# Performance work log

Measured on AMD Instinct MI355X. Metric: run time of the kernel, lower is better.

Reference implementation:

```python
import jax, jax.numpy as jnp
import numpy as np

B, S, D, H = 4, 2048, 1024, 16
DEPTH = D // H


def setup_inputs() -> dict:
    key = jax.random.key(0)
    ks = jax.random.split(key, 11)
    s = 1.0 / np.sqrt(D)
    return {
        "q": jax.random.normal(ks[0], (B, S, D), jnp.float32),
        "k": jax.random.normal(ks[1], (B, S, D), jnp.float32),
        "v": jax.random.normal(ks[2], (B, S, D), jnp.float32),
        "wq": jax.random.normal(ks[3], (D, D), jnp.float32) * s,
        "bq": jnp.zeros((D,), jnp.float32),
        "wk": jax.random.normal(ks[4], (D, D), jnp.float32) * s,
        "bk": jnp.zeros((D,), jnp.float32),
        "wv": jax.random.normal(ks[5], (D, D), jnp.float32) * s,
        "bv": jnp.zeros((D,), jnp.float32),
        "wo": jax.random.normal(ks[6], (D, D), jnp.float32) * s,
        "bo": jnp.zeros((D,), jnp.float32),
    }


def _split_heads(x):
    # [B,S,D] -> [B,H,S,depth]
    b, s, _ = x.shape
    return x.reshape(b, s, H, DEPTH).transpose(0, 2, 1, 3)


def reference(q, k, v, wq, bq, wk, bk, wv, bv, wo, bo):
    qh = _split_heads(q @ wq + bq)
    kh = _split_heads(k @ wk + bk)
    vh = _split_heads(v @ wv + bv)
    scale = 1.0 / jnp.sqrt(jnp.asarray(DEPTH, jnp.float32))
    logits = jnp.einsum("bhsd,bhtd->bhst", qh, kh) * scale  # [B,H,S,S]
    attn = jax.nn.softmax(logits, axis=-1)
    out = jnp.einsum("bhst,bhtd->bhsd", attn, vh)
    out = out.transpose(0, 2, 1, 3).reshape(q.shape[0], -1, D)
    return out @ wo + bo
```

## Files before the change

### kernel.cpp

```cpp
#include <hip/hip_runtime.h>
#include <hip/hip_bf16.h>

#define BATCH 4
#define SEQ   2048
#define DIM   1024
#define NHEAD 16
#define HDIM  64

typedef __bf16    bf16x8 __attribute__((ext_vector_type(8)));
typedef float     f32x16 __attribute__((ext_vector_type(16)));
typedef unsigned  u32;

__device__ __forceinline__ unsigned short f2bfu(float x) {
  union { __hip_bfloat16 b; unsigned short u; } c; c.b = __float2bfloat16(x); return c.u;
}
__device__ __forceinline__ u32 cvtpk(float lo, float hi) {
  u32 r; asm("v_cvt_pk_bf16_f32 %0, %1, %2" : "=v"(r) : "v"(lo), "v"(hi)); return r;
}
__device__ __forceinline__ int swz4(int row) {
  return ((row & 7) ^ ((row >> 3) & 7)) << 2;
}

#define GLDS16(GP, LP)                                                         \
  __builtin_amdgcn_global_load_lds(                                            \
      (const __attribute__((address_space(1))) void*)(GP),                     \
      (__attribute__((address_space(3))) void*)(LP), 16, 0, 0)

__global__ __launch_bounds__(256)
void wtrans(const float* __restrict__ w0, const float* __restrict__ w1,
            const float* __restrict__ w2,
            __hip_bfloat16* __restrict__ t0, __hip_bfloat16* __restrict__ t1,
            __hip_bfloat16* __restrict__ t2)
{
  __shared__ float T[64][68];
  const int mat  = blockIdx.x >> 8;
  const int tile = blockIdx.x & 255;
  const float* W = mat == 0 ? w0 : (mat == 1 ? w1 : w2);
  __hip_bfloat16* Wt = mat == 0 ? t0 : (mat == 1 ? t1 : t2);
  const int k0 = (tile >> 4) * 64, n0 = (tile & 15) * 64;
  const int tid = threadIdx.x;
  const int r = tid >> 2, cq = (tid & 3) * 16;
  #pragma unroll
  for (int j = 0; j < 4; ++j) {
    const float4 v = *reinterpret_cast<const float4*>(&W[(size_t)(k0 + r) * DIM + n0 + cq + j * 4]);
    T[r][cq + j * 4 + 0] = v.x; T[r][cq + j * 4 + 1] = v.y;
    T[r][cq + j * 4 + 2] = v.z; T[r][cq + j * 4 + 3] = v.w;
  }
  __syncthreads();
  u32 o[8];
  #pragma unroll
  for (int j = 0; j < 8; ++j)
    o[j] = cvtpk(T[cq + 2 * j][r], T[cq + 2 * j + 1][r]);
  *reinterpret_cast<uint4*>(&Wt[(size_t)(n0 + r) * DIM + k0 + cq + 0]) = make_uint4(o[0], o[1], o[2], o[3]);
  *reinterpret_cast<uint4*>(&Wt[(size_t)(n0 + r) * DIM + k0 + cq + 8]) = make_uint4(o[4], o[5], o[6], o[7]);
}

template<typename TIN, typename TOUT, int NSEG>
__global__ __launch_bounds__(256, 2)
void gemm2ph(const TIN* __restrict__ A0, const TIN* __restrict__ A1, const TIN* __restrict__ A2,
             const __hip_bfloat16* __restrict__ W0, const __hip_bfloat16* __restrict__ W1,
             const __hip_bfloat16* __restrict__ W2,
             const float* __restrict__ b0, const float* __restrict__ b1, const float* __restrict__ b2,
             TOUT* __restrict__ C0, TOUT* __restrict__ C1, TOUT* __restrict__ C2)
{
  __shared__ __align__(16) u32 As32[2][128][32];
  __shared__ __align__(16) u32 Bs32[2][128][32];

  constexpr bool AF32 = (sizeof(TIN) == 4);
  constexpr int K = 1024, NT = 16;

  const int seg = (NSEG == 1) ? 0 : (blockIdx.x >> 9);
  const int idb = (NSEG == 1) ? blockIdx.x : (blockIdx.x & 511);
  const TIN* A = seg == 0 ? A0 : (seg == 1 ? A1 : A2);
  const __hip_bfloat16* Wt = seg == 0 ? W0 : (seg == 1 ? W1 : W2);
  const float* bias = seg == 0 ? b0 : (seg == 1 ? b1 : b2);
  TOUT* C = seg == 0 ? C0 : (seg == 1 ? C1 : C2);

  const int xcd = idb & 7, rr = idb >> 3;
  const int bx = rr & 7, by = xcd + 8 * (rr >> 3);
  const int m0 = by * 128, n0 = bx * 128;

  const int tid = threadIdx.x, lane = tid & 63, w = tid >> 6;
  const int l31 = lane & 31, hi = lane >> 5;
  const int wm = w >> 1, wn = w & 1;

  f32x16 acc[2][2] = {};

  const __hip_bfloat16* bptr[4];
  #pragma unroll
  for (int i = 0; i < 4; ++i) {
    const int off = (w * 4 + i) * 1024 + lane * 16;
    const int r = off >> 7;
    const int s = (off >> 4) & 7;
    bptr[i] = Wt + (size_t)(n0 + r) * K + (s ^ (r & 7)) * 8;
  }
  const TIN* aptr[4];
  const int arow = tid >> 3;
  const int acb  = (tid & 7) * 8;
  #pragma unroll
  for (int i = 0; i < 4; ++i) {
    if constexpr (!AF32) {
      const int off = (w * 4 + i) * 1024 + lane * 16;
      const int r = off >> 7;
      const int s = (off >> 4) & 7;
      aptr[i] = A + (size_t)(m0 + r) * K + (s ^ (r & 7)) * 8;
    } else {
      aptr[i] = nullptr;
    }
  }

  float4 ar[4][2];

  auto loadA_f32 = [&](int t) {
    #pragma unroll
    for (int p = 0; p < 4; ++p) {
      const float* ap = (const float*)A + (size_t)(m0 + arow + p * 32) * K + t * 64 + acb;
      ar[p][0] = *reinterpret_cast<const float4*>(ap);
      ar[p][1] = *reinterpret_cast<const float4*>(ap + 4);
    }
  };
  auto writeA_f32 = [&](int nxt) {
    #pragma unroll
    for (int p = 0; p < 4; ++p) {
      const int row = arow + p * 32;
      uint4 pk;
      pk.x = cvtpk(ar[p][0].x, ar[p][0].y);
      pk.y = cvtpk(ar[p][0].z, ar[p][0].w);
      pk.z = cvtpk(ar[p][1].x, ar[p][1].y);
      pk.w = cvtpk(ar[p][1].z, ar[p][1].w);
      *reinterpret_cast<uint4*>(&As32[nxt][row][((tid & 7) * 4) ^ ((row & 7) << 2)]) = pk;
    }
  };
  auto stageA_bf = [&](int nxt, int t) {
    #pragma unroll
    for (int i = 0; i < 4; ++i)
      GLDS16((const __hip_bfloat16*)aptr[i] + t * 64,
             (char*)As32 + nxt * 16384 + (w * 4 + i) * 1024);
  };
  auto stageB = [&](int nxt, int t) {
    #pragma unroll
    for (int i = 0; i < 4; ++i)
      GLDS16(bptr[i] + t * 64,
             (char*)Bs32 + nxt * 16384 + (w * 4 + i) * 1024);
  };

  int aoff[4][2], boff[4][2];
  #pragma unroll
  for (int kk = 0; kk < 4; ++kk) {
    #pragma unroll
    for (int mi = 0; mi < 2; ++mi) {
      const int r = wm * 64 + mi * 32 + l31;
      aoff[kk][mi] = r * 128 + (((kk * 2 + hi) ^ (r & 7)) << 4);
    }
    #pragma unroll
    for (int ni = 0; ni < 2; ++ni) {
      const int c = wn * 64 + ni * 32 + l31;
      boff[kk][ni] = c * 128 + (((kk * 2 + hi) ^ (c & 7)) << 4);
    }
  }

  if constexpr (AF32) { loadA_f32(0); writeA_f32(0); }
  else                { stageA_bf(0, 0); }
  stageB(0, 0);
  __syncthreads();

  for (int t = 0; t < NT; ++t) {
    const int cur = t & 1, nxt = cur ^ 1;

    if (t + 1 < NT) {
      if constexpr (AF32) loadA_f32(t + 1);
      else                stageA_bf(nxt, t + 1);
      stageB(nxt, t + 1);
    }

    const char* ab = (const char*)As32 + cur * 16384;
    const char* bb = (const char*)Bs32 + cur * 16384;
    #pragma unroll
    for (int kk = 0; kk < 4; ++kk) {
      bf16x8 af[2], bfv[2];
      #pragma unroll
      for (int mi = 0; mi < 2; ++mi)
        af[mi] = *reinterpret_cast<const bf16x8*>(ab + aoff[kk][mi]);
      #pragma unroll
      for (int ni = 0; ni < 2; ++ni)
        bfv[ni] = *reinterpret_cast<const bf16x8*>(bb + boff[kk][ni]);
      __builtin_amdgcn_s_setprio(1);
      #pragma unroll
      for (int mi = 0; mi < 2; ++mi)
        #pragma unroll
        for (int ni = 0; ni < 2; ++ni)
          acc[mi][ni] = __builtin_amdgcn_mfma_f32_32x32x16_bf16(af[mi], bfv[ni], acc[mi][ni], 0, 0, 0);
      __builtin_amdgcn_s_setprio(0);
    }

    if (t + 1 < NT) {
      if constexpr (AF32) writeA_f32(nxt);
    }
    __syncthreads();
  }

  #pragma unroll
  for (int ni = 0; ni < 2; ++ni) {
    const int col = n0 + wn * 64 + ni * 32 + l31;
    const float bv = bias[col];
    #pragma unroll
    for (int mi = 0; mi < 2; ++mi) {
      #pragma unroll
      for (int g = 0; g < 4; ++g)
        #pragma unroll
        for (int e = 0; e < 4; ++e) {
          const int row = m0 + wm * 64 + mi * 32 + g * 8 + hi * 4 + e;
          const float val = acc[mi][ni][g * 4 + e] + bv;
          if constexpr (sizeof(TOUT) == 2)
            C[(size_t)row * DIM + col] = __float2bfloat16(val);
          else
            C[(size_t)row * DIM + col] = val;
        }
    }
  }
}

__global__ __launch_bounds__(256, 2)
void flash_attn(const __hip_bfloat16* __restrict__ Qb,
                const __hip_bfloat16* __restrict__ Kb,
                const __hip_bfloat16* __restrict__ Vb,
                __hip_bfloat16* __restrict__ Ob)
{
  __shared__ __align__(16) u32 Ks32[2][64][32];
  __shared__ __align__(16) u32 Vt32[2][64][32];

  const int id  = blockIdx.x;
  const int xcd = id & 7;
  const int r_  = id >> 3;
  const int qb  = r_ & 7;
  const int hh  = (r_ >> 3) & 1;
  const int b   = r_ >> 4;
  const int h   = xcd + 8 * hh;

  const int tid = threadIdx.x, lane = tid & 63, wv = tid >> 6;
  const int l31 = lane & 31, hi = lane >> 5;

  const size_t headoff = (size_t)h * HDIM;
  const int q0 = b * SEQ + qb * 256 + wv * 64;

  bf16x8 qf[2][4];
  #pragma unroll
  for (int qh = 0; qh < 2; ++qh)
    #pragma unroll
    for (int dk = 0; dk < 4; ++dk)
      qf[qh][dk] = *reinterpret_cast<const bf16x8*>(
        &Qb[(size_t)(q0 + qh * 32 + l31) * DIM + headoff + dk * 16 + hi * 8]);

  f32x16 accO[2][2] = {};
  float l_run[2] = {0.f, 0.f};

  const int skey = tid >> 2;
  const int sdq  = tid & 3;
  const int vkp  = tid >> 3;
  const int vdb  = tid & 7;
  const size_t kbase = (size_t)b * SEQ * DIM + headoff;

  uint4 kst[2], vst[2];
  auto load_t = [&](int t) {
    const int kb = t * 64;
    const __hip_bfloat16* kp_ = &Kb[kbase + (size_t)(kb + skey) * DIM + sdq * 16];
    kst[0] = *reinterpret_cast<const uint4*>(kp_);
    kst[1] = *reinterpret_cast<const uint4*>(kp_ + 8);
    const __hip_bfloat16* vp_ = &Vb[kbase + (size_t)(kb + vkp * 2) * DIM + vdb * 8];
    vst[0] = *reinterpret_cast<const uint4*>(vp_);
    vst[1] = *reinterpret_cast<const uint4*>(vp_ + DIM);
  };
  auto store_t = [&](int bb) {
    const int sk = swz4(skey);
    *reinterpret_cast<uint4*>(&Ks32[bb][skey][(sdq * 8 + 0) ^ sk]) = kst[0];
    *reinterpret_cast<uint4*>(&Ks32[bb][skey][(sdq * 8 + 4) ^ sk]) = kst[1];
    const unsigned short* a  = (const unsigned short*)&vst[0];
    const unsigned short* bv = (const unsigned short*)&vst[1];
    #pragma unroll
    for (int j = 0; j < 8; ++j) {
      const int row = vdb * 8 + j;
      Vt32[bb][row][vkp ^ swz4(row)] = (u32)a[j] | ((u32)bv[j] << 16);
    }
  };

  load_t(0); store_t(0); __syncthreads();

  const float C1 = 0.125f * 1.44269504f;

  for (int t = 0; t < SEQ / 64; ++t) {
    const int bb = t & 1;
    if (t < SEQ / 64 - 1) load_t(t + 1);

    f32x16 sacc[2][2] = {};
    __builtin_amdgcn_s_setprio(1);
    #pragma unroll
    for (int kt = 0; kt < 2; ++kt) {
      const int row = kt * 32 + l31;
      const int sk = swz4(row);
      #pragma unroll
      for (int dk = 0; dk < 4; ++dk) {
        bf16x8 kf = *reinterpret_cast<const bf16x8*>(&Ks32[bb][row][(dk * 8 + hi * 4) ^ sk]);
        sacc[0][kt] = __builtin_amdgcn_mfma_f32_32x32x16_bf16(kf, qf[0][dk], sacc[0][kt], 0, 0, 0);
        sacc[1][kt] = __builtin_amdgcn_mfma_f32_32x32x16_bf16(kf, qf[1][dk], sacc[1][kt], 0, 0, 0);
      }
    }
    __builtin_amdgcn_s_setprio(0);

    u32 pf[2][4][4];
    #pragma unroll
    for (int qh = 0; qh < 2; ++qh) {
      #pragma unroll
      for (int kt = 0; kt < 2; ++kt)
        #pragma unroll
        for (int r2 = 0; r2 < 16; ++r2)
          sacc[qh][kt][r2] = __builtin_amdgcn_exp2f(sacc[qh][kt][r2] * C1);

      f32x16 ps = sacc[qh][0] + sacc[qh][1];
      float s8[8];
      #pragma unroll
      for (int i = 0; i < 8; ++i) s8[i] = ps[i] + ps[i + 8];
      float rs = ((s8[0] + s8[1]) + (s8[2] + s8[3])) + ((s8[4] + s8[5]) + (s8[6] + s8[7]));
      rs += __shfl_xor(rs, 32);
      l_run[qh] += rs;

#define MAKE_PF(DST, P, B) do {                                            \
      u32 x1 = cvtpk(P[B+0], P[B+1]);                                      \
      u32 y1 = cvtpk(P[B+4], P[B+5]);                                      \
      u32 x2 = cvtpk(P[B+2], P[B+3]);                                      \
      u32 y2 = cvtpk(P[B+6], P[B+7]);                                      \
      auto s1 = __builtin_amdgcn_permlane32_swap(x1, y1, false, false);    \
      auto s2 = __builtin_amdgcn_permlane32_swap(x2, y2, false, false);    \
      DST[0] = (u32)s1[0]; DST[1] = (u32)s2[0];                            \
      DST[2] = (u32)s1[1]; DST[3] = (u32)s2[1];                            \
    } while (0)
      MAKE_PF(pf[qh][0], sacc[qh][0], 0);
      MAKE_PF(pf[qh][1], sacc[qh][0], 8);
      MAKE_PF(pf[qh][2], sacc[qh][1], 0);
      MAKE_PF(pf[qh][3], sacc[qh][1], 8);
#undef MAKE_PF
    }

    __builtin_amdgcn_s_setprio(1);
    #pragma unroll
    for (int dt = 0; dt < 2; ++dt) {
      const int row = dt * 32 + l31;
      const int sk = swz4(row);
      #pragma unroll
      for (int kf = 0; kf < 4; ++kf) {
        bf16x8 vf = *reinterpret_cast<const bf16x8*>(&Vt32[bb][row][(kf * 8 + hi * 4) ^ sk]);
        #pragma unroll
        for (int qh = 0; qh < 2; ++qh) {
          union { u32 u[4]; bf16x8 v; } pu;
          pu.u[0] = pf[qh][kf][0]; pu.u[1] = pf[qh][kf][1];
          pu.u[2] = pf[qh][kf][2]; pu.u[3] = pf[qh][kf][3];
          accO[qh][dt] = __builtin_amdgcn_mfma_f32_32x32x16_bf16(vf, pu.v, accO[qh][dt], 0, 0, 0);
        }
      }
    }
    __builtin_amdgcn_s_setprio(0);

    if (t < SEQ / 64 - 1) store_t(bb ^ 1);
    __syncthreads();
  }

  #pragma unroll
  for (int qh = 0; qh < 2; ++qh) {
    const float inv = 1.f / l_run[qh];
    const size_t rowbase = (size_t)(q0 + qh * 32 + l31) * DIM + headoff;
    #pragma unroll
    for (int dt = 0; dt < 2; ++dt)
      #pragma unroll
      for (int g = 0; g < 4; ++g) {
        ushort4 o;
        o.x = f2bfu(accO[qh][dt][g * 4 + 0] * inv);
        o.y = f2bfu(accO[qh][dt][g * 4 + 1] * inv);
        o.z = f2bfu(accO[qh][dt][g * 4 + 2] * inv);
        o.w = f2bfu(accO[qh][dt][g * 4 + 3] * inv);
        *reinterpret_cast<ushort4*>(&Ob[rowbase + dt * 32 + g * 8 + hi * 4]) = o;
      }
  }
}

extern "C" void kernel_launch(void* const* d_in, const int* in_sizes, int n_in,
                              void* d_out, int out_size, void* d_ws, size_t ws_size,
                              hipStream_t stream)
{
  const float* q  = (const float*)d_in[0];
  const float* k  = (const float*)d_in[1];
  const float* v  = (const float*)d_in[2];
  const float* wq = (const float*)d_in[3];
  const float* bq = (const float*)d_in[4];
  const float* wk = (const float*)d_in[5];
  const float* bk = (const float*)d_in[6];
  const float* wv = (const float*)d_in[7];
  const float* bv = (const float*)d_in[8];
  const float* wo = (const float*)d_in[9];
  const float* bo = (const float*)d_in[10];

  const size_t MN = (size_t)BATCH * SEQ * DIM;
  const size_t KK = (size_t)DIM * DIM;

  __hip_bfloat16* Qb = (__hip_bfloat16*)d_ws;
  __hip_bfloat16* Kb = Qb + MN;
  __hip_bfloat16* Vb = Kb + MN;
  __hip_bfloat16* S3 = Vb + MN;
  __hip_bfloat16* WtQ = S3;
  __hip_bfloat16* WtK = S3 + KK;
  __hip_bfloat16* WtV = S3 + 2 * KK;
  __hip_bfloat16* Ob  = S3;
  __hip_bfloat16* WtO = (__hip_bfloat16*)d_ws;

  wtrans<<<768, 256, 0, stream>>>(wq, wk, wv, WtQ, WtK, WtV);

  gemm2ph<float, __hip_bfloat16, 3><<<1536, 256, 0, stream>>>(
      q, k, v, WtQ, WtK, WtV, bq, bk, bv, Qb, Kb, Vb);

  flash_attn<<<512, 256, 0, stream>>>(Qb, Kb, Vb, Ob);

  wtrans<<<256, 256, 0, stream>>>(wo, wo, wo, WtO, WtO, WtO);

  gemm2ph<__hip_bfloat16, float, 1><<<512, 256, 0, stream>>>(
      Ob, Ob, Ob, WtO, WtO, WtO, bo, bo, bo,
      (float*)d_out, (float*)d_out, (float*)d_out);
}
```

Measured before the change: 208.1 us.

## Replace double-buffered GEMM LDS staging with single buffer and extra barrier

The projection GEMM drops its two-stage LDS ping-pong and uses one shared buffer for A and B. After each k-tile's MFMAs, a barrier is taken, the next tile is staged (direct-to-LDS loads for bf16 and B, convert-and-store for fp32 A), and a second barrier follows. This halves LDS use, which could allow more resident blocks. It gives up the overlap of global loads with MFMA compute and adds a barrier per iteration, so loads are now exposed.

```diff
diff --git a/kernel.cpp b/kernel.cpp
--- a/kernel.cpp
+++ b/kernel.cpp
@@ -57,14 +57,14 @@
 
 template<typename TIN, typename TOUT, int NSEG>
 __global__ __launch_bounds__(256, 2)
-void gemm2ph(const TIN* __restrict__ A0, const TIN* __restrict__ A1, const TIN* __restrict__ A2,
+void gemm1ph(const TIN* __restrict__ A0, const TIN* __restrict__ A1, const TIN* __restrict__ A2,
              const __hip_bfloat16* __restrict__ W0, const __hip_bfloat16* __restrict__ W1,
              const __hip_bfloat16* __restrict__ W2,
              const float* __restrict__ b0, const float* __restrict__ b1, const float* __restrict__ b2,
              TOUT* __restrict__ C0, TOUT* __restrict__ C1, TOUT* __restrict__ C2)
 {
-  __shared__ __align__(16) u32 As32[2][128][32];
-  __shared__ __align__(16) u32 Bs32[2][128][32];
+  __shared__ __align__(16) u32 As32[128][32];
+  __shared__ __align__(16) u32 Bs32[128][32];
 
   constexpr bool AF32 = (sizeof(TIN) == 4);
   constexpr int K = 1024, NT = 16;
@@ -119,7 +119,7 @@
       ar[p][1] = *reinterpret_cast<const float4*>(ap + 4);
     }
   };
-  auto writeA_f32 = [&](int nxt) {
+  auto writeA_f32 = [&]() {
     #pragma unroll
     for (int p = 0; p < 4; ++p) {
       const int row = arow + p * 32;
@@ -128,20 +128,18 @@
       pk.y = cvtpk(ar[p][0].z, ar[p][0].w);
       pk.z = cvtpk(ar[p][1].x, ar[p][1].y);
       pk.w = cvtpk(ar[p][1].z, ar[p][1].w);
-      *reinterpret_cast<uint4*>(&As32[nxt][row][((tid & 7) * 4) ^ ((row & 7) << 2)]) = pk;
-    }
-  };
-  auto stageA_bf = [&](int nxt, int t) {
+      *reinterpret_cast<uint4*>(&As32[row][((tid & 7) * 4) ^ ((row & 7) << 2)]) = pk;
+    }
+  };
+  auto stageA_bf = [&](int t) {
     #pragma unroll
     for (int i = 0; i < 4; ++i)
-      GLDS16((const __hip_bfloat16*)aptr[i] + t * 64,
-             (char*)As32 + nxt * 16384 + (w * 4 + i) * 1024);
-  };
-  auto stageB = [&](int nxt, int t) {
+      GLDS16((const __hip_bfloat16*)aptr[i] + t * 64, (char*)As32 + (w * 4 + i) * 1024);
+  };
+  auto stageB = [&](int t) {
     #pragma unroll
     for (int i = 0; i < 4; ++i)
-      GLDS16(bptr[i] + t * 64,
-             (char*)Bs32 + nxt * 16384 + (w * 4 + i) * 1024);
+      GLDS16(bptr[i] + t * 64, (char*)Bs32 + (w * 4 + i) * 1024);
   };
 
   int aoff[4][2], boff[4][2];
@@ -159,31 +157,23 @@
     }
   }
 
-  if constexpr (AF32) { loadA_f32(0); writeA_f32(0); }
-  else                { stageA_bf(0, 0); }
-  stageB(0, 0);
+  if constexpr (AF32) { loadA_f32(0); writeA_f32(); }
+  else                { stageA_bf(0); }
+  stageB(0);
   __syncthreads();
 
   for (int t = 0; t < NT; ++t) {
-    const int cur = t & 1, nxt = cur ^ 1;
-
-    if (t + 1 < NT) {
-      if constexpr (AF32) loadA_f32(t + 1);
-      else                stageA_bf(nxt, t + 1);
-      stageB(nxt, t + 1);
-    }
-
-    const char* ab = (const char*)As32 + cur * 16384;
-    const char* bb = (const char*)Bs32 + cur * 16384;
+    if (t + 1 < NT) { if constexpr (AF32) loadA_f32(t + 1); }
+
     #pragma unroll
     for (int kk = 0; kk < 4; ++kk) {
       bf16x8 af[2], bfv[2];
       #pragma unroll
       for (int mi = 0; mi < 2; ++mi)
-        af[mi] = *reinterpret_cast<const bf16x8*>(ab + aoff[kk][mi]);
+        af[mi] = *reinterpret_cast<const bf16x8*>((const char*)As32 + aoff[kk][mi]);
       #pragma unroll
       for (int ni = 0; ni < 2; ++ni)
-        bfv[ni] = *reinterpret_cast<const bf16x8*>(bb + boff[kk][ni]);
+        bfv[ni] = *reinterpret_cast<const bf16x8*>((const char*)Bs32 + boff[kk][ni]);
       __builtin_amdgcn_s_setprio(1);
       #pragma unroll
       for (int mi = 0; mi < 2; ++mi)
@@ -192,11 +182,14 @@
           acc[mi][ni] = __builtin_amdgcn_mfma_f32_32x32x16_bf16(af[mi], bfv[ni], acc[mi][ni], 0, 0, 0);
       __builtin_amdgcn_s_setprio(0);
     }
+    __syncthreads();
 
     if (t + 1 < NT) {
-      if constexpr (AF32) writeA_f32(nxt);
-    }
-    __syncthreads();
+      if constexpr (AF32) writeA_f32();
+      else                stageA_bf(t + 1);
+      stageB(t + 1);
+      __syncthreads();
+    }
   }
 
   #pragma unroll
@@ -412,14 +405,14 @@
 
   wtrans<<<768, 256, 0, stream>>>(wq, wk, wv, WtQ, WtK, WtV);
 
-  gemm2ph<float, __hip_bfloat16, 3><<<1536, 256, 0, stream>>>(
+  gemm1ph<float, __hip_bfloat16, 3><<<1536, 256, 0, stream>>>(
       q, k, v, WtQ, WtK, WtV, bq, bk, bv, Qb, Kb, Vb);
 
   flash_attn<<<512, 256, 0, stream>>>(Qb, Kb, Vb, Ob);
 
   wtrans<<<256, 256, 0, stream>>>(wo, wo, wo, WtO, WtO, WtO);
 
-  gemm2ph<__hip_bfloat16, float, 1><<<512, 256, 0, stream>>>(
+  gemm1ph<__hip_bfloat16, float, 1><<<512, 256, 0, stream>>>(
       Ob, Ob, Ob, WtO, WtO, WtO, bo, bo, bo,
       (float*)d_out, (float*)d_out, (float*)d_out);
 }
```

After: 200.8 us. -3.5%, faster.
